# Kernel tuning notes

Measured on AMD Instinct MI355X. Metric: run time of the kernel, lower is better.

## Reference

```python
import jax, jax.numpy as jnp
import numpy as np

DIM = 768
HEADS = 8
EPS = 1e-6


def _layernorm(x, gamma, beta):
    # torch: mean over last dim; std with Bessel correction (unbiased, ddof=1)
    mean = jnp.mean(x, axis=-1, keepdims=True)
    std = jnp.std(x, axis=-1, keepdims=True, ddof=1)
    return gamma * (x - mean) / (std + EPS) + beta


def setup_inputs() -> dict:
    key = jax.random.key(0)
    ks = jax.random.split(key, 8)
    s = 0.02
    return {
        "x": jax.random.normal(ks[0], (16384, DIM), dtype=jnp.float32),
        "wq_w": jax.random.normal(ks[1], (DIM, DIM), dtype=jnp.float32) * s,
        "wq_b": jnp.zeros((DIM,), dtype=jnp.float32),
        "wk_w": jax.random.normal(ks[2], (DIM, DIM), dtype=jnp.float32) * s,
        "wk_b": jnp.zeros((DIM,), dtype=jnp.float32),
        "wv_w": jax.random.normal(ks[3], (DIM, DIM), dtype=jnp.float32) * s,
        "wv_b": jnp.zeros((DIM,), dtype=jnp.float32),
        "d1_w": jax.random.normal(ks[4], (4 * DIM, DIM), dtype=jnp.float32) * s,
        "d1_b": jnp.zeros((4 * DIM,), dtype=jnp.float32),
        "d2_w": jax.random.normal(ks[5], (DIM, 4 * DIM), dtype=jnp.float32) * s,
        "d2_b": jnp.zeros((DIM,), dtype=jnp.float32),
        "g1": jnp.ones((1,), dtype=jnp.float32),
        "b1": jnp.zeros((1,), dtype=jnp.float32),
        "g2": jnp.ones((1,), dtype=jnp.float32),
        "b2": jnp.zeros((1,), dtype=jnp.float32),
    }


def reference(x, wq_w, wq_b, wk_w, wk_b, wv_w, wv_b,
              d1_w, d1_b, d2_w, d2_b, g1, b1, g2, b2):
    T = x.shape[0]
    # --- pre-LN + attention ---
    xn = _layernorm(x, g1, b1)                      # [T, D]
    q = xn @ wq_w.T + wq_b                          # [T, D]
    k = xn @ wk_w.T + wk_b
    v = xn @ wv_w.T + wv_b
    # faithful to q.view(-1, num_heads, key_dim): groups of HEADS tokens
    q = q.reshape(T // HEADS, HEADS, DIM)
    k = k.reshape(T // HEADS, HEADS, DIM)
    v = v.reshape(T // HEADS, HEADS, DIM)
    scores = jnp.einsum('ghd,gkd->ghk', q, k) / jnp.sqrt(jnp.float32(DIM))
    attn_w = jax.nn.softmax(scores, axis=-1)        # [T/8, 8, 8]
    attn = jnp.einsum('ghk,gkd->ghd', attn_w, v).reshape(T, DIM)
    x = attn + x
    # --- pre-LN + MLP ---
    xn = _layernorm(x, g2, b2)
    h = jax.nn.gelu(xn @ d1_w.T + d1_b, approximate=False)  # [T, 4D]
    x = (h @ d2_w.T + d2_b) + x
    return x
```

## Files before the change

kernel.cpp:

```cpp
#include <hip/hip_runtime.h>
#include <stdint.h>

#define DIM 768
#define HDIM 3072

typedef unsigned short u16;
typedef unsigned char u8;
typedef __bf16 bf16x8 __attribute__((ext_vector_type(8)));
typedef float f32x4 __attribute__((ext_vector_type(4)));
typedef float f32x16 __attribute__((ext_vector_type(16)));
typedef int i32x8 __attribute__((ext_vector_type(8)));

__device__ __forceinline__ float b2f(u16 u) {
    union { unsigned i; float f; } v; v.i = ((unsigned)u) << 16; return v.f;
}
__device__ __forceinline__ u16 f2b(float f) {
    union { float f; unsigned i; } v; v.f = f;
    unsigned r = (v.i + 0x7FFFu + ((v.i >> 16) & 1u)) >> 16;
    return (u16)r;
}
__device__ __forceinline__ float gelu_f(float v) {
    float u = v * (1.5957691216f + 0.07135481627f * v * v);
    float e = __builtin_amdgcn_exp2f(-1.442695041f * u);
    return v * __builtin_amdgcn_rcpf(1.0f + e);
}
__device__ __forceinline__ void gl_lds16(const void* g, void* l) {
    __builtin_amdgcn_global_load_lds(
        (__attribute__((address_space(1))) void*)(g),
        (__attribute__((address_space(3))) void*)(l), 16, 0, 0);
}

__global__ __launch_bounds__(256) void cvt_bf16(const float4* __restrict__ s,
                                                ushort4* __restrict__ d, int n4) {
    int i = blockIdx.x * 256 + threadIdx.x;
    if (i < n4) {
        float4 v = s[i];
        ushort4 o;
        o.x = f2b(v.x); o.y = f2b(v.y); o.z = f2b(v.z); o.w = f2b(v.w);
        d[i] = o;
    }
}

__global__ __launch_bounds__(256) void cvt_fp8(const float4* __restrict__ s,
                                               unsigned* __restrict__ d, int n4) {
    int i = blockIdx.x * 256 + threadIdx.x;
    if (i < n4) {
        float4 v = s[i];
        int p = __builtin_amdgcn_cvt_pk_fp8_f32(v.x, v.y, 0, false);
        p = __builtin_amdgcn_cvt_pk_fp8_f32(v.z, v.w, p, true);
        d[i] = (unsigned)p;
    }
}

__global__ void pack_bias3(const float* __restrict__ a, const float* __restrict__ b,
                           const float* __restrict__ c, float* __restrict__ o) {
    int i = blockIdx.x * 256 + threadIdx.x;
    if (i < DIM) { o[i] = a[i]; o[i + DIM] = b[i]; o[i + 2 * DIM] = c[i]; }
}

__global__ __launch_bounds__(256) void ln_rows_f8(const float* __restrict__ x, u8* __restrict__ xn,
                                                  const float* __restrict__ g, const float* __restrict__ b) {
    int row = blockIdx.x * 4 + (threadIdx.x >> 6);
    int lane = threadIdx.x & 63;
    const float* xr = x + (size_t)row * DIM + lane * 12;
    float v[12];
#pragma unroll
    for (int i = 0; i < 3; ++i) {
        float4 t = ((const float4*)xr)[i];
        v[i * 4 + 0] = t.x; v[i * 4 + 1] = t.y; v[i * 4 + 2] = t.z; v[i * 4 + 3] = t.w;
    }
    float s = 0.f, ss = 0.f;
#pragma unroll
    for (int i = 0; i < 12; ++i) { s += v[i]; ss += v[i] * v[i]; }
#pragma unroll
    for (int o = 32; o; o >>= 1) { s += __shfl_xor(s, o); ss += __shfl_xor(ss, o); }
    float mean = s * (1.f / DIM);
    float var = (ss - (float)DIM * mean * mean) * (1.f / (DIM - 1));
    float denom = sqrtf(var) + 1e-6f;
    float sc = g[0] / denom, bb = b[0] - mean * sc;
    unsigned* outp = (unsigned*)(xn + (size_t)row * DIM + lane * 12);
#pragma unroll
    for (int i = 0; i < 3; ++i) {
        int p = __builtin_amdgcn_cvt_pk_fp8_f32(v[i * 4 + 0] * sc + bb, v[i * 4 + 1] * sc + bb, 0, false);
        p = __builtin_amdgcn_cvt_pk_fp8_f32(v[i * 4 + 2] * sc + bb, v[i * 4 + 3] * sc + bb, p, true);
        outp[i] = (unsigned)p;
    }
}

template <int EPI>
__global__ __launch_bounds__(256)
void gemm_f8(const u8* __restrict__ A, const u8* __restrict__ B,
             const float* __restrict__ bias, const float* __restrict__ resid,
             u16* __restrict__ Cb, float* __restrict__ Cf, int N, int K) {
    __shared__ __align__(16) u8 As[128 * 128];
    __shared__ __align__(16) u8 Bs[128 * 128];
    const int tid = threadIdx.x, lane = tid & 63, wave = tid >> 6;
    const int row0 = blockIdx.x * 128, col0 = blockIdx.y * 128;
    const int wm = (wave >> 1) * 64, wn = (wave & 1) * 64;
    f32x16 acc[2][2] = {};

    const int srow = lane >> 3;
    const int schunk = ((lane & 7) ^ srow) * 16;
    const u8* Ag = A + (size_t)(row0 + wave * 8 + srow) * K + schunk;
    const u8* Bg = B + (size_t)(col0 + wave * 8 + srow) * K + schunk;
    const size_t s32 = (size_t)32 * K;
    u8* AsW = As + wave * 1024;
    u8* BsW = Bs + wave * 1024;

    const int r31 = lane & 31, khalf = lane >> 5;

    for (int kb = 0; kb < K; kb += 128) {
#pragma unroll
        for (int i = 0; i < 4; ++i) {
            gl_lds16(Ag + i * s32, AsW + i * 4096);
            gl_lds16(Bg + i * s32, BsW + i * 4096);
        }
        Ag += 128; Bg += 128;
        __syncthreads();
#pragma unroll
        for (int ks = 0; ks < 2; ++ks) {
            const int c0 = ks * 4 + khalf * 2;
            union { i32x8 v; uint4 q[2]; } af[2], bfr[2];
#pragma unroll
            for (int ib = 0; ib < 2; ++ib) {
                const int r = wm + ib * 32 + r31;
                const u8* base = As + r * 128;
                const int x7 = (r & 7);
                af[ib].q[0] = *(const uint4*)(base + ((c0 ^ x7) * 16));
                af[ib].q[1] = *(const uint4*)(base + (((c0 + 1) ^ x7) * 16));
            }
#pragma unroll
            for (int jb = 0; jb < 2; ++jb) {
                const int r = wn + jb * 32 + r31;
                const u8* base = Bs + r * 128;
                const int x7 = (r & 7);
                bfr[jb].q[0] = *(const uint4*)(base + ((c0 ^ x7) * 16));
                bfr[jb].q[1] = *(const uint4*)(base + (((c0 + 1) ^ x7) * 16));
            }
#pragma unroll
            for (int ib = 0; ib < 2; ++ib)
#pragma unroll
                for (int jb = 0; jb < 2; ++jb)
                    acc[ib][jb] = __builtin_amdgcn_mfma_scale_f32_32x32x64_f8f6f4(
                        af[ib].v, bfr[jb].v, acc[ib][jb], 0, 0,
                        0, 0x7F7F7F7F, 0, 0x7F7F7F7F);
        }
        __syncthreads();
    }
    const int colq = col0 + wn + r31;
    const int rbase = row0 + wm + 4 * khalf;
#pragma unroll
    for (int jb = 0; jb < 2; ++jb) {
        const int col = colq + jb * 32;
        const float bv = bias[col];
#pragma unroll
        for (int ib = 0; ib < 2; ++ib) {
#pragma unroll
            for (int reg = 0; reg < 16; ++reg) {
                const int row = rbase + ib * 32 + (reg & 3) + 8 * (reg >> 2);
                float v = acc[ib][jb][reg] + bv;
                size_t idx = (size_t)row * N + col;
                if (EPI == 2) Cf[idx] = v + resid[idx];
                else          Cb[idx] = f2b(v);
            }
        }
    }
}

__global__ __launch_bounds__(256)
void gemm_up(const u16* __restrict__ A, const u16* __restrict__ B,
             const float* __restrict__ bias, u8* __restrict__ C8, int N, int K) {
    __shared__ __align__(16) u16 As[128 * 64];
    __shared__ __align__(16) u16 Bs[128 * 64];
    const int tid = threadIdx.x;
    const int row0 = blockIdx.x * 128, col0 = blockIdx.y * 128;
    const int lane = tid & 63, wave = tid >> 6;
    const int wm = (wave >> 1) * 64, wn = (wave & 1) * 64;
    const int la = lane & 15, qd = lane >> 4;
    f32x4 acc[4][4] = {};

    const int srow = lane >> 3;
    const int schunk = (lane & 7) ^ srow;
    const u16* Ag = A + (size_t)(row0 + wave * 8 + srow) * K + schunk * 8;
    const u16* Bg = B + (size_t)(col0 + wave * 8 + srow) * K + schunk * 8;
    const size_t s32 = (size_t)32 * K;
    u16* AsW = &As[wave * 512];
    u16* BsW = &Bs[wave * 512];
    const int x7 = la & 7;

    for (int kb = 0; kb < K; kb += 64) {
#pragma unroll
        for (int i = 0; i < 4; ++i) {
            gl_lds16(Ag + i * s32, AsW + i * 2048);
            gl_lds16(Bg + i * s32, BsW + i * 2048);
        }
        Ag += 64; Bg += 64;
        __syncthreads();
#pragma unroll
        for (int ks = 0; ks < 2; ++ks) {
            const int cp = ((ks * 4 + qd) ^ x7) * 8;
            bf16x8 af[4], bfr[4];
#pragma unroll
            for (int i = 0; i < 4; ++i)
                af[i] = *(const bf16x8*)(&As[(wm + i * 16 + la) * 64 + cp]);
#pragma unroll
            for (int j = 0; j < 4; ++j)
                bfr[j] = *(const bf16x8*)(&Bs[(wn + j * 16 + la) * 64 + cp]);
#pragma unroll
            for (int i = 0; i < 4; ++i)
#pragma unroll
                for (int j = 0; j < 4; ++j)
                    acc[i][j] = __builtin_amdgcn_mfma_f32_16x16x32_bf16(af[i], bfr[j], acc[i][j], 0, 0, 0);
        }
        __syncthreads();
    }
    const int rb = row0 + wm + qd * 4;
    const int cb = col0 + wn + la;
#pragma unroll
    for (int j = 0; j < 4; ++j) {
        const int col = cb + j * 16;
        const float bv = bias[col];
#pragma unroll
        for (int i = 0; i < 4; ++i) {
#pragma unroll
            for (int r = 0; r < 4; ++r) {
                const int row = rb + i * 16 + r;
                float v = gelu_f(acc[i][j][r] + bv);
                int p = __builtin_amdgcn_cvt_pk_fp8_f32(v, v, 0, false);
                C8[(size_t)row * N + col] = (u8)(p & 0xFF);
            }
        }
    }
}

__global__ __launch_bounds__(256)
void attn_ln(const u16* __restrict__ qkv, const float* __restrict__ x,
             float* __restrict__ x1, u16* __restrict__ xn2,
             const float* __restrict__ g, const float* __restrict__ b) {
    __shared__ __align__(16) u16 sq[8 * 2304];
    __shared__ float sw[64];
    const int tid = threadIdx.x;
    const size_t gbase = (size_t)blockIdx.x * (8 * 2304);
    const uint4* src = (const uint4*)(qkv + gbase);
    uint4* dst = (uint4*)sq;
#pragma unroll
    for (int i = 0; i < 9; ++i) dst[tid + i * 256] = src[tid + i * 256];
    __syncthreads();
    const int wave = tid >> 6, lane = tid & 63;
#pragma unroll 1
    for (int p = wave * 16; p < wave * 16 + 16; ++p) {
        const u16* qr = sq + (p >> 3) * 2304;
        const u16* kr = sq + (p & 7) * 2304 + 768;
        float s = 0.f;
#pragma unroll
        for (int i = 0; i < 12; ++i) { int d = lane + i * 64; s += b2f(qr[d]) * b2f(kr[d]); }
#pragma unroll
        for (int o = 32; o; o >>= 1) s += __shfl_xor(s, o);
        if (lane == 0) sw[p] = s;
    }
    __syncthreads();
    if (tid < 8) {
        const float scl = 0.03608439182435161f;
        float e[8]; float m = -1e30f;
#pragma unroll
        for (int j = 0; j < 8; ++j) m = fmaxf(m, sw[tid * 8 + j]);
        float sum = 0.f;
#pragma unroll
        for (int j = 0; j < 8; ++j) { e[j] = expf((sw[tid * 8 + j] - m) * scl); sum += e[j]; }
        float inv = 1.f / sum;
#pragma unroll
        for (int j = 0; j < 8; ++j) sw[tid * 8 + j] = e[j] * inv;
    }
    __syncthreads();
    const int h = tid >> 5, li = tid & 31;
    float w[8];
#pragma unroll
    for (int kk = 0; kk < 8; ++kk) w[kk] = sw[h * 8 + kk];
    const size_t trow = (size_t)blockIdx.x * 8 + h;
    const float* xr = x + trow * DIM;
    float* x1r = x1 + trow * DIM;
    u16* xnr = xn2 + trow * DIM;
    float xv[24], s = 0.f, ss = 0.f;
#pragma unroll
    for (int i = 0; i < 24; ++i) {
        int d = li + i * 32;
        float o = 0.f;
#pragma unroll
        for (int kk = 0; kk < 8; ++kk) o += w[kk] * b2f(sq[kk * 2304 + 1536 + d]);
        float val = o + xr[d];
        x1r[d] = val;
        xv[i] = val; s += val; ss += val * val;
    }
#pragma unroll
    for (int o2 = 16; o2; o2 >>= 1) { s += __shfl_xor(s, o2); ss += __shfl_xor(ss, o2); }
    float mean = s * (1.f / 768.f);
    float var = (ss - 768.f * mean * mean) * (1.f / 767.f);
    float denom = sqrtf(var) + 1e-6f;
    float sc = g[0] / denom, bb = b[0] - mean * sc;
#pragma unroll
    for (int i = 0; i < 24; ++i) xnr[li + i * 32] = f2b(xv[i] * sc + bb);
}

extern "C" void kernel_launch(void* const* d_in, const int* in_sizes, int n_in,
                              void* d_out, int out_size, void* d_ws, size_t ws_size,
                              hipStream_t stream) {
    (void)n_in; (void)out_size; (void)ws_size;
    const float* x    = (const float*)d_in[0];
    const float* wq_w = (const float*)d_in[1];
    const float* wq_b = (const float*)d_in[2];
    const float* wk_w = (const float*)d_in[3];
    const float* wk_b = (const float*)d_in[4];
    const float* wv_w = (const float*)d_in[5];
    const float* wv_b = (const float*)d_in[6];
    const float* d1_w = (const float*)d_in[7];
    const float* d1_b = (const float*)d_in[8];
    const float* d2_w = (const float*)d_in[9];
    const float* d2_b = (const float*)d_in[10];
    const float* g1 = (const float*)d_in[11];
    const float* b1 = (const float*)d_in[12];
    const float* g2 = (const float*)d_in[13];
    const float* b2 = (const float*)d_in[14];
    float* out = (float*)d_out;
    char* ws = (char*)d_ws;

    const int T = in_sizes[0] / DIM;

    u8*    w_qkv8 = (u8*)(ws);
    u16*   w_d1   = (u16*)(ws + 1769472);
    u8*    w_d28  = (u8*)(ws + 6488064);
    float* b_qkv  = (float*)(ws + 8847360);
    u16*   xn2    = (u16*)(ws + 8856576);
    float* x1     = (float*)(ws + 34022400);
    u8*    xn1_8  = (u8*)(ws + 34022400);
    u16*   qkv    = (u16*)(ws + 84354048);
    u8*    h8     = (u8*)(ws + 84354048);

    cvt_fp8<<<576, 256, 0, stream>>>((const float4*)wq_w, (unsigned*)w_qkv8, 147456);
    cvt_fp8<<<576, 256, 0, stream>>>((const float4*)wk_w, (unsigned*)(w_qkv8 + 589824), 147456);
    cvt_fp8<<<576, 256, 0, stream>>>((const float4*)wv_w, (unsigned*)(w_qkv8 + 1179648), 147456);
    cvt_bf16<<<2304, 256, 0, stream>>>((const float4*)d1_w, (ushort4*)w_d1, 589824);
    cvt_fp8<<<2304, 256, 0, stream>>>((const float4*)d2_w, (unsigned*)w_d28, 589824);
    pack_bias3<<<3, 256, 0, stream>>>(wq_b, wk_b, wv_b, b_qkv);

    ln_rows_f8<<<T / 4, 256, 0, stream>>>(x, xn1_8, g1, b1);
    gemm_f8<0><<<dim3(T / 128, 18), 256, 0, stream>>>(xn1_8, w_qkv8, b_qkv, nullptr, qkv, nullptr, 2304, 768);
    attn_ln<<<T / 8, 256, 0, stream>>>(qkv, x, x1, xn2, g2, b2);
    gemm_up<<<dim3(T / 128, 24), 256, 0, stream>>>(xn2, w_d1, d1_b, h8, 3072, 768);
    gemm_f8<2><<<dim3(T / 128, 6), 256, 0, stream>>>(h8, w_d28, d2_b, x1, nullptr, out, 768, 3072);
}
```

Baseline: 402.3 us.

## Swap MFMA operands for row-contiguous epilogues and vectorize attention loads/stores

Swaps the A/B operands of the MFMA calls in both GEMMs so each lane's accumulator registers hold consecutive columns of one row. The epilogues can then write packed bf16/fp8 or float4 values and read the bias and residual as float4, instead of scattered single-element stores. The attention+LN kernel is also changed to read q/k/v and x with vector loads and to write x1 and xn2 in 16-byte chunks. GEMM N/K become template constants. This targets the uncoalesced scalar global stores in the epilogues, at the cost of more registers and more complex indexing.

```diff
diff --git a/kernel.cpp b/kernel.cpp
--- a/kernel.cpp
+++ b/kernel.cpp
@@ -7,6 +7,7 @@
 typedef unsigned short u16;
 typedef unsigned char u8;
 typedef __bf16 bf16x8 __attribute__((ext_vector_type(8)));
+typedef __bf16 bf16x4 __attribute__((ext_vector_type(4)));
 typedef float f32x4 __attribute__((ext_vector_type(4)));
 typedef float f32x16 __attribute__((ext_vector_type(16)));
 typedef int i32x8 __attribute__((ext_vector_type(8)));
@@ -18,6 +19,9 @@
     union { float f; unsigned i; } v; v.f = f;
     unsigned r = (v.i + 0x7FFFu + ((v.i >> 16) & 1u)) >> 16;
     return (u16)r;
+}
+__device__ __forceinline__ unsigned pack2b(float a, float b) {
+    return (unsigned)f2b(a) | ((unsigned)f2b(b) << 16);
 }
 __device__ __forceinline__ float gelu_f(float v) {
     float u = v * (1.5957691216f + 0.07135481627f * v * v);
@@ -87,11 +91,11 @@
     }
 }
 
-template <int EPI>
+template <int EPI, int N, int K>
 __global__ __launch_bounds__(256)
 void gemm_f8(const u8* __restrict__ A, const u8* __restrict__ B,
              const float* __restrict__ bias, const float* __restrict__ resid,
-             u16* __restrict__ Cb, float* __restrict__ Cf, int N, int K) {
+             u16* __restrict__ Cb, float* __restrict__ Cf) {
     __shared__ __align__(16) u8 As[128 * 128];
     __shared__ __align__(16) u8 Bs[128 * 128];
     const int tid = threadIdx.x, lane = tid & 63, wave = tid >> 6;
@@ -142,34 +146,42 @@
 #pragma unroll
                 for (int jb = 0; jb < 2; ++jb)
                     acc[ib][jb] = __builtin_amdgcn_mfma_scale_f32_32x32x64_f8f6f4(
-                        af[ib].v, bfr[jb].v, acc[ib][jb], 0, 0,
+                        bfr[jb].v, af[ib].v, acc[ib][jb], 0, 0,
                         0, 0x7F7F7F7F, 0, 0x7F7F7F7F);
         }
         __syncthreads();
     }
-    const int colq = col0 + wn + r31;
-    const int rbase = row0 + wm + 4 * khalf;
-#pragma unroll
-    for (int jb = 0; jb < 2; ++jb) {
-        const int col = colq + jb * 32;
-        const float bv = bias[col];
-#pragma unroll
-        for (int ib = 0; ib < 2; ++ib) {
-#pragma unroll
-            for (int reg = 0; reg < 16; ++reg) {
-                const int row = rbase + ib * 32 + (reg & 3) + 8 * (reg >> 2);
-                float v = acc[ib][jb][reg] + bv;
-                size_t idx = (size_t)row * N + col;
-                if (EPI == 2) Cf[idx] = v + resid[idx];
-                else          Cb[idx] = f2b(v);
+#pragma unroll
+    for (int ib = 0; ib < 2; ++ib) {
+        const int row = row0 + wm + ib * 32 + r31;
+#pragma unroll
+        for (int jb = 0; jb < 2; ++jb) {
+#pragma unroll
+            for (int gq = 0; gq < 4; ++gq) {
+                const int cb = col0 + wn + jb * 32 + gq * 8 + 4 * khalf;
+                float4 bv = *(const float4*)(bias + cb);
+                float v0 = acc[ib][jb][gq * 4 + 0] + bv.x;
+                float v1 = acc[ib][jb][gq * 4 + 1] + bv.y;
+                float v2 = acc[ib][jb][gq * 4 + 2] + bv.z;
+                float v3 = acc[ib][jb][gq * 4 + 3] + bv.w;
+                const size_t idx = (size_t)row * N + cb;
+                if (EPI == 2) {
+                    float4 rv = *(const float4*)(resid + idx);
+                    float4 o; o.x = v0 + rv.x; o.y = v1 + rv.y; o.z = v2 + rv.z; o.w = v3 + rv.w;
+                    *(float4*)(Cf + idx) = o;
+                } else {
+                    uint2 o; o.x = pack2b(v0, v1); o.y = pack2b(v2, v3);
+                    *(uint2*)(Cb + idx) = o;
+                }
             }
         }
     }
 }
 
+template <int N, int K>
 __global__ __launch_bounds__(256)
 void gemm_up(const u16* __restrict__ A, const u16* __restrict__ B,
-             const float* __restrict__ bias, u8* __restrict__ C8, int N, int K) {
+             const float* __restrict__ bias, u8* __restrict__ C8) {
     __shared__ __align__(16) u16 As[128 * 64];
     __shared__ __align__(16) u16 Bs[128 * 64];
     const int tid = threadIdx.x;
@@ -210,25 +222,24 @@
             for (int i = 0; i < 4; ++i)
 #pragma unroll
                 for (int j = 0; j < 4; ++j)
-                    acc[i][j] = __builtin_amdgcn_mfma_f32_16x16x32_bf16(af[i], bfr[j], acc[i][j], 0, 0, 0);
+                    acc[i][j] = __builtin_amdgcn_mfma_f32_16x16x32_bf16(bfr[j], af[i], acc[i][j], 0, 0, 0);
         }
         __syncthreads();
     }
-    const int rb = row0 + wm + qd * 4;
-    const int cb = col0 + wn + la;
-#pragma unroll
-    for (int j = 0; j < 4; ++j) {
-        const int col = cb + j * 16;
-        const float bv = bias[col];
-#pragma unroll
-        for (int i = 0; i < 4; ++i) {
-#pragma unroll
-            for (int r = 0; r < 4; ++r) {
-                const int row = rb + i * 16 + r;
-                float v = gelu_f(acc[i][j][r] + bv);
-                int p = __builtin_amdgcn_cvt_pk_fp8_f32(v, v, 0, false);
-                C8[(size_t)row * N + col] = (u8)(p & 0xFF);
-            }
+#pragma unroll
+    for (int i = 0; i < 4; ++i) {
+        const int row = row0 + wm + i * 16 + la;
+#pragma unroll
+        for (int j = 0; j < 4; ++j) {
+            const int cb = col0 + wn + j * 16 + qd * 4;
+            float4 bv = *(const float4*)(bias + cb);
+            float v0 = gelu_f(acc[i][j][0] + bv.x);
+            float v1 = gelu_f(acc[i][j][1] + bv.y);
+            float v2 = gelu_f(acc[i][j][2] + bv.z);
+            float v3 = gelu_f(acc[i][j][3] + bv.w);
+            int p = __builtin_amdgcn_cvt_pk_fp8_f32(v0, v1, 0, false);
+            p = __builtin_amdgcn_cvt_pk_fp8_f32(v2, v3, p, true);
+            *(unsigned*)(C8 + (size_t)row * N + cb) = (unsigned)p;
         }
     }
 }
@@ -247,13 +258,19 @@
     for (int i = 0; i < 9; ++i) dst[tid + i * 256] = src[tid + i * 256];
     __syncthreads();
     const int wave = tid >> 6, lane = tid & 63;
-#pragma unroll 1
+#pragma unroll 2
     for (int p = wave * 16; p < wave * 16 + 16; ++p) {
         const u16* qr = sq + (p >> 3) * 2304;
         const u16* kr = sq + (p & 7) * 2304 + 768;
+        bf16x8 qa = *(const bf16x8*)(qr + lane * 8);
+        bf16x8 ka = *(const bf16x8*)(kr + lane * 8);
+        bf16x4 qb = *(const bf16x4*)(qr + 512 + lane * 4);
+        bf16x4 kb = *(const bf16x4*)(kr + 512 + lane * 4);
         float s = 0.f;
 #pragma unroll
-        for (int i = 0; i < 12; ++i) { int d = lane + i * 64; s += b2f(qr[d]) * b2f(kr[d]); }
+        for (int i = 0; i < 8; ++i) s += (float)qa[i] * (float)ka[i];
+#pragma unroll
+        for (int i = 0; i < 4; ++i) s += (float)qb[i] * (float)kb[i];
 #pragma unroll
         for (int o = 32; o; o >>= 1) s += __shfl_xor(s, o);
         if (lane == 0) sw[p] = s;
@@ -279,17 +296,31 @@
     const size_t trow = (size_t)blockIdx.x * 8 + h;
     const float* xr = x + trow * DIM;
     float* x1r = x1 + trow * DIM;
-    u16* xnr = xn2 + trow * DIM;
     float xv[24], s = 0.f, ss = 0.f;
 #pragma unroll
-    for (int i = 0; i < 24; ++i) {
-        int d = li + i * 32;
-        float o = 0.f;
-#pragma unroll
-        for (int kk = 0; kk < 8; ++kk) o += w[kk] * b2f(sq[kk * 2304 + 1536 + d]);
-        float val = o + xr[d];
-        x1r[d] = val;
-        xv[i] = val; s += val; ss += val * val;
+    for (int wd = 0; wd < 3; ++wd) {
+        const int d0 = wd * 256 + li * 8;
+        float o[8] = {};
+#pragma unroll
+        for (int kk = 0; kk < 8; ++kk) {
+            bf16x8 vv = *(const bf16x8*)(sq + kk * 2304 + 1536 + d0);
+#pragma unroll
+            for (int e = 0; e < 8; ++e) o[e] += w[kk] * (float)vv[e];
+        }
+        float4 xa = *(const float4*)(xr + d0);
+        float4 xb = *(const float4*)(xr + d0 + 4);
+        float vals[8] = { o[0] + xa.x, o[1] + xa.y, o[2] + xa.z, o[3] + xa.w,
+                          o[4] + xb.x, o[5] + xb.y, o[6] + xb.z, o[7] + xb.w };
+        float4 w0, w1;
+        w0.x = vals[0]; w0.y = vals[1]; w0.z = vals[2]; w0.w = vals[3];
+        w1.x = vals[4]; w1.y = vals[5]; w1.z = vals[6]; w1.w = vals[7];
+        *(float4*)(x1r + d0) = w0;
+        *(float4*)(x1r + d0 + 4) = w1;
+#pragma unroll
+        for (int e = 0; e < 8; ++e) {
+            xv[wd * 8 + e] = vals[e];
+            s += vals[e]; ss += vals[e] * vals[e];
+        }
     }
 #pragma unroll
     for (int o2 = 16; o2; o2 >>= 1) { s += __shfl_xor(s, o2); ss += __shfl_xor(ss, o2); }
@@ -297,8 +328,17 @@
     float var = (ss - 768.f * mean * mean) * (1.f / 767.f);
     float denom = sqrtf(var) + 1e-6f;
     float sc = g[0] / denom, bb = b[0] - mean * sc;
-#pragma unroll
-    for (int i = 0; i < 24; ++i) xnr[li + i * 32] = f2b(xv[i] * sc + bb);
+    u16* xnr = xn2 + trow * DIM;
+#pragma unroll
+    for (int wd = 0; wd < 3; ++wd) {
+        const int d0 = wd * 256 + li * 8;
+        uint4 o;
+        o.x = pack2b(xv[wd * 8 + 0] * sc + bb, xv[wd * 8 + 1] * sc + bb);
+        o.y = pack2b(xv[wd * 8 + 2] * sc + bb, xv[wd * 8 + 3] * sc + bb);
+        o.z = pack2b(xv[wd * 8 + 4] * sc + bb, xv[wd * 8 + 5] * sc + bb);
+        o.w = pack2b(xv[wd * 8 + 6] * sc + bb, xv[wd * 8 + 7] * sc + bb);
+        *(uint4*)(xnr + d0) = o;
+    }
 }
 
 extern "C" void kernel_launch(void* const* d_in, const int* in_sizes, int n_in,
@@ -343,8 +383,8 @@
     pack_bias3<<<3, 256, 0, stream>>>(wq_b, wk_b, wv_b, b_qkv);
 
     ln_rows_f8<<<T / 4, 256, 0, stream>>>(x, xn1_8, g1, b1);
-    gemm_f8<0><<<dim3(T / 128, 18), 256, 0, stream>>>(xn1_8, w_qkv8, b_qkv, nullptr, qkv, nullptr, 2304, 768);
+    gemm_f8<0, 2304, 768><<<dim3(T / 128, 18), 256, 0, stream>>>(xn1_8, w_qkv8, b_qkv, nullptr, qkv, nullptr);
     attn_ln<<<T / 8, 256, 0, stream>>>(qkv, x, x1, xn2, g2, b2);
-    gemm_up<<<dim3(T / 128, 24), 256, 0, stream>>>(xn2, w_d1, d1_b, h8, 3072, 768);
-    gemm_f8<2><<<dim3(T / 128, 6), 256, 0, stream>>>(h8, w_d28, d2_b, x1, nullptr, out, 768, 3072);
-}
+    gemm_up<3072, 768><<<dim3(T / 128, 24), 256, 0, stream>>>(xn2, w_d1, d1_b, h8);
+    gemm_f8<2, 768, 3072><<<dim3(T / 128, 6), 256, 0, stream>>>(h8, w_d28, d2_b, x1, nullptr, out);
+}
```

Result: slower. 416.7 us (+3.6%).
